# Performance work log

Measured on AMD Instinct MI355X. Metric: run time of the kernel, lower is better.

Reference implementation:

```python
import jax, jax.numpy as jnp
import numpy as np
from jax import lax

# Static pair index table: all C(135,2)=9045 unordered node pairs (replaces the
# nested Python loops with a single gather).
PAIR_I, PAIR_J = np.triu_indices(135, k=1)
RRELU_SLOPE = (1.0 / 8.0 + 1.0 / 3.0) / 2.0  # eval-mode RReLU negative slope
BN_SCALE = 1.0 / float(np.sqrt(1.0 + 1e-5))  # eval BN with running mean=0, var=1


def _leaky(x):
    return jnp.where(x > 0, x, 0.01 * x)


def _conv1d(x, w, b):
    # x: (N, Cin, L), w: (Cout, Cin, K) -> (N, Cout, L-K+1), VALID
    y = lax.conv_general_dilated(x, w, (1,), 'VALID',
                                 dimension_numbers=('NCH', 'OIH', 'NCH'))
    return y + b[None, :, None]


def _bn_eval(x, g, b):
    # nn.BatchNorm1d in eval with fresh running stats (mean=0, var=1)
    return x * (g * BN_SCALE)[None, :, None] + b[None, :, None]


def _maxpool2d(x):
    # nn.MaxPool2d(2) applied to a 3D (N, H, W) tensor: 2x2 pool over (H, W)
    return lax.reduce_window(x, -jnp.inf, lax.max, (1, 2, 2), (1, 2, 2), 'VALID')


def setup_inputs() -> dict:
    key = jax.random.key(0)
    ks = iter(jax.random.split(key, 40))

    def w(shape, scale=0.05):
        return (jax.random.normal(next(ks), shape, jnp.float32) * scale)

    inp = {
        'x': jax.random.normal(next(ks), (30, 135, 375), jnp.float32),
        # FeatureExtractor
        'conv1_w': w((32, 1, 3)), 'conv1_b': jnp.zeros((32,), jnp.float32),
        'bn1_g': jnp.ones((32,), jnp.float32), 'bn1_b': jnp.zeros((32,), jnp.float32),
        'conv2_w': w((64, 16, 3)), 'conv2_b': jnp.zeros((64,), jnp.float32),
        'bn2_g': jnp.ones((64,), jnp.float32), 'bn2_b': jnp.zeros((64,), jnp.float32),
        'conv3_w': w((96, 32, 3)), 'conv3_b': jnp.zeros((96,), jnp.float32),
        'bn3_g': jnp.ones((96,), jnp.float32), 'bn3_b': jnp.zeros((96,), jnp.float32),
        'fe_fc_w': w((48 * 45, 32)), 'fe_fc_b': jnp.zeros((32,), jnp.float32),
        # SimilarityMeasureNetwork
        'sim_w1': w((64, 32)), 'sim_b1': jnp.zeros((32,), jnp.float32),
        'sim_w2': w((32, 16)), 'sim_b2': jnp.zeros((16,), jnp.float32),
        'sim_w3': w((16, 8)), 'sim_b3': jnp.zeros((8,), jnp.float32),
        'sim_w4': w((8, 1)), 'sim_b4': jnp.zeros((1,), jnp.float32),
        # ClassificationNet(9045, 3)
        'cls_w1': w((9045, 1024), 0.01), 'cls_b1': jnp.zeros((1024,), jnp.float32),
        'cls_w2': w((1024, 256)), 'cls_b2': jnp.zeros((256,), jnp.float32),
        'cls_w3': w((256, 64)), 'cls_b3': jnp.zeros((64,), jnp.float32),
        'cls_w4': w((64, 3)), 'cls_b4': jnp.zeros((3,), jnp.float32),
    }
    return inp


def reference(x, conv1_w, conv1_b, bn1_g, bn1_b, conv2_w, conv2_b, bn2_g, bn2_b,
              conv3_w, conv3_b, bn3_g, bn3_b, fe_fc_w, fe_fc_b,
              sim_w1, sim_b1, sim_w2, sim_b2, sim_w3, sim_b3, sim_w4, sim_b4,
              cls_w1, cls_b1, cls_w2, cls_b2, cls_w3, cls_b3, cls_w4, cls_b4):
    B = x.shape[0]  # 30 subjects
    h = x.reshape(B * 135, 1, 375)
    # FeatureExtractor (all subjects*nodes batched together)
    h = _maxpool2d(_leaky(_bn_eval(_conv1d(h, conv1_w, conv1_b), bn1_g, bn1_b)))  # (N,16,186)
    h = _maxpool2d(_leaky(_bn_eval(_conv1d(h, conv2_w, conv2_b), bn2_g, bn2_b)))  # (N,32,92)
    h = _maxpool2d(_leaky(_bn_eval(_conv1d(h, conv3_w, conv3_b), bn3_g, bn3_b)))  # (N,48,45)
    h = h.reshape(B * 135, -1) @ fe_fc_w + fe_fc_b  # (B*135, 32)
    feats = h.reshape(B, 135, 32)

    # All-pairs concat: single gather replacing the nested loops -> (B, 9045, 64)
    pi = jnp.asarray(PAIR_I)
    pj = jnp.asarray(PAIR_J)
    pairs = jnp.concatenate([feats[:, pi, :], feats[:, pj, :]], axis=-1)

    # SimilarityMeasureNetwork
    s = jax.nn.relu(pairs @ sim_w1 + sim_b1)
    s = jax.nn.relu(s @ sim_w2 + sim_b2)
    s = jax.nn.relu(s @ sim_w3 + sim_b3)
    s = jnp.tanh(s @ sim_w4 + sim_b4)  # (B, 9045, 1)
    subjects = s[..., 0]  # (B, 9045)

    # ClassificationNet (eval mode: RReLU -> fixed slope, dropout -> identity)
    c = subjects @ cls_w1 + cls_b1
    c = jnp.where(c >= 0, c, RRELU_SLOPE * c)
    c = jax.nn.relu(c @ cls_w2 + cls_b2)
    c = jax.nn.relu(c @ cls_w3 + cls_b3)
    c = c @ cls_w4 + cls_b4
    return jax.nn.log_softmax(c, axis=1)  # (B, 3)
```

## Files before the change

kernel.cpp:

```cpp
#include <hip/hip_runtime.h>
#include <math.h>

#define BN_SCALE 0.99999500003749967f
#define RRELU_SLOPE 0.22916666666666666f

static __device__ __forceinline__ float leaky(float v) { return v > 0.f ? v : 0.01f * v; }

typedef __attribute__((ext_vector_type(8))) short bf16x8;
typedef __attribute__((ext_vector_type(4))) float f32x4;
typedef __attribute__((ext_vector_type(4))) unsigned u32x4;

static __device__ __forceinline__ unsigned short f2bf(float f) {
  unsigned u = __builtin_bit_cast(unsigned, f);
  u = (u + 0x7FFFu + ((u >> 16) & 1u)) >> 16;
  return (unsigned short)u;
}

__global__ __launch_bounds__(256) void setup_kernel(
    const float* __restrict__ w2c, const float* __restrict__ g2,
    const float* __restrict__ w3c, const float* __restrict__ g3,
    const float* __restrict__ fcw, const float* __restrict__ fcb,
    const float* __restrict__ w1,  const float* __restrict__ b1,
    unsigned short* __restrict__ w2frag,
    unsigned short* __restrict__ w3frag,
    unsigned short* __restrict__ bfragGG,
    float* __restrict__ bgagb,
    unsigned short* __restrict__ subjectsA)
{
  const int item = blockIdx.x * 256 + threadIdx.x;
  if (item < 512) {
    const int tl = item >> 6, lane = item & 63;
    const int mt = tl >> 1, kc = tl & 1;
    const int lr = lane & 15, quad = lane >> 4;
    const int c = mt * 16 + lr;
    const float gs = g2[c] * BN_SCALE;
#pragma unroll
    for (int j = 0; j < 8; ++j) {
      const int k = quad * 8 + j;
      float v;
      if (kc == 0) { const int tap = k >> 4, ci = k & 15; v = w2c[c * 48 + ci * 3 + tap] * gs; }
      else         { v = (k < 16) ? w2c[c * 48 + k * 3 + 2] * gs : 0.f; }
      w2frag[item * 8 + j] = f2bf(v);
    }
  } else if (item < 1664) {
    const int it = item - 512;
    const int tl = it >> 6, lane = it & 63;
    const int mt = tl / 3, tap = tl - mt * 3;
    const int lr = lane & 15, quad = lane >> 4;
    const int c = mt * 16 + lr;
    const float gs = g3[c] * BN_SCALE;
#pragma unroll
    for (int j = 0; j < 8; ++j) {
      const int ci = quad * 8 + j;
      w3frag[it * 8 + j] = f2bf(w3c[c * 96 + ci * 3 + tap] * gs);
    }
  } else if (item < 19072) {
    const int it = item - 1664;
    const int chunk = it >> 8;
    const int rem = it & 255;
    const int nt = rem >> 6;
    const int lane = rem & 63;
    const int lr = lane & 15, quad = lane >> 4;
    const int n = nt * 16 + lr;
    const int off = (n >= 32) ? 32 : 0;
    const int nj = n & 31;
    float w1col[32];
#pragma unroll 8
    for (int q = 0; q < 32; ++q) w1col[q] = w1[(q + off) * 32 + nj];
#pragma unroll
    for (int j = 0; j < 8; ++j) {
      const int k = chunk * 32 + quad * 8 + j;
      float v = 0.f;
      if (k < 2160) {
        const float* fr = fcw + (size_t)k * 32;
#pragma unroll 8
        for (int q = 0; q < 32; ++q) v = fmaf(fr[q], w1col[q], v);
      }
      bfragGG[(size_t)it * 8 + j] = f2bf(v);
    }
  } else if (item < 19136) {
    const int n = item - 19072;
    const int off = (n >= 32) ? 32 : 0;
    const int nj = n & 31;
    float s = (n < 32) ? b1[nj] : 0.f;
    for (int q = 0; q < 32; ++q) s = fmaf(fcb[q], w1[(q + off) * 32 + nj], s);
    bgagb[n] = s;
  } else if (item < 55360) {
    const int idx = item - 19136;
    uint4 z = {0u, 0u, 0u, 0u};
    ((uint4*)subjectsA)[idx] = z;
  }
}

__global__ __launch_bounds__(64) void fe_kernel(
    const float* __restrict__ x,
    const float* __restrict__ w1c, const float* __restrict__ b1c,
    const float* __restrict__ g1,  const float* __restrict__ bb1,
    const float* __restrict__ b2c, const float* __restrict__ g2, const float* __restrict__ bb2,
    const float* __restrict__ b3c, const float* __restrict__ g3, const float* __restrict__ bb3,
    const unsigned short* __restrict__ w2frag,
    const unsigned short* __restrict__ w3frag,
    unsigned short* __restrict__ act3)
{
  __shared__ __align__(16) char A[8448];
  const int lane = threadIdx.x;
  const int quad = lane >> 4, lr = lane & 15;
  const int n = blockIdx.x;

  unsigned short* buf = (unsigned short*)A;
  float* be2 = (float*)(A + 6272);
  float* be3 = (float*)(A + 6528);
  float* sx  = (float*)(A + 6912);

  const float* xr = x + (size_t)n * 375;
  for (int i = lane; i < 375; i += 64) sx[i] = xr[i];

  bf16x8 a2[4][2];
#pragma unroll
  for (int mt = 0; mt < 4; ++mt)
#pragma unroll
    for (int kc = 0; kc < 2; ++kc)
      a2[mt][kc] = *(const bf16x8*)(w2frag + ((mt * 2 + kc) * 64 + lane) * 8);

  be2[lane] = b2c[lane] * (g2[lane] * BN_SCALE) + bb2[lane];
  be3[lane] = b3c[lane] * (g3[lane] * BN_SCALE) + bb3[lane];
  if (lane < 32) be3[64 + lane] = b3c[64 + lane] * (g3[64 + lane] * BN_SCALE) + bb3[64 + lane];
  ((unsigned*)buf)[1488 + lane] = 0;

  const int cp = lane & 7;
  float u[4][3], bbr[4];
#pragma unroll
  for (int d = 0; d < 4; ++d) {
    const int c = cp * 4 + d;
    const float gs = g1[c] * BN_SCALE;
    u[d][0] = w1c[c * 3 + 0] * gs;
    u[d][1] = w1c[c * 3 + 1] * gs;
    u[d][2] = w1c[c * 3 + 2] * gs;
    bbr[d] = b1c[c] * gs + bb1[c];
  }

  for (int o = lane; o < 1488; o += 64) {
    const int l = o >> 3;
    const int p = 2 * l;
    const float x0 = sx[p], x1 = sx[p + 1], x2 = sx[p + 2], x3 = sx[p + 3];
    unsigned pk = 0;
#pragma unroll
    for (int uu = 0; uu < 2; ++uu) {
      float m = -3.4e38f;
#pragma unroll
      for (int dc = 0; dc < 2; ++dc) {
        const int d = uu * 2 + dc;
        const float v0 = fmaf(x0, u[d][0], fmaf(x1, u[d][1], fmaf(x2, u[d][2], bbr[d])));
        const float v1 = fmaf(x1, u[d][0], fmaf(x2, u[d][1], fmaf(x3, u[d][2], bbr[d])));
        m = fmaxf(m, fmaxf(v0, v1));
      }
      pk |= (unsigned)f2bf(leaky(m)) << (16 * uu);
    }
    ((unsigned*)buf)[l * 8 + cp] = pk;
  }

  float be2r[4][4];
#pragma unroll
  for (int mt = 0; mt < 4; ++mt)
#pragma unroll
    for (int r = 0; r < 4; ++r) be2r[mt][r] = be2[mt * 16 + quad * 4 + r];

#pragma unroll 2
  for (int nt = 0; nt < 12; ++nt) {
    const int nrow = nt * 16 + lr;
    bf16x8 b0 = *(const bf16x8*)(buf + (nrow + (quad >> 1)) * 16 + (quad & 1) * 8);
    bf16x8 b1 = *(const bf16x8*)(buf + (nrow + 2) * 16 + (quad & 1) * 8);
    f32x4 acc[4];
#pragma unroll
    for (int mt = 0; mt < 4; ++mt)
#pragma unroll
      for (int r = 0; r < 4; ++r) acc[mt][r] = be2r[mt][r];
#pragma unroll
    for (int mt = 0; mt < 4; ++mt)
      acc[mt] = __builtin_amdgcn_mfma_f32_16x16x32_bf16(a2[mt][0], b0, acc[mt], 0, 0, 0);
#pragma unroll
    for (int mt = 0; mt < 4; ++mt)
      acc[mt] = __builtin_amdgcn_mfma_f32_16x16x32_bf16(a2[mt][1], b1, acc[mt], 0, 0, 0);
#pragma unroll
    for (int mt = 0; mt < 4; ++mt) {
      float o[4];
#pragma unroll
      for (int r = 0; r < 4; ++r)
        o[r] = fmaxf(acc[mt][r], __shfl_xor(acc[mt][r], 1));
      if ((lr & 1) == 0) {
        const int np = nrow >> 1;
        if (np <= 91) {
          const float m0 = leaky(fmaxf(o[0], o[1]));
          const float m1 = leaky(fmaxf(o[2], o[3]));
          const unsigned pk = (unsigned)f2bf(m0) | ((unsigned)f2bf(m1) << 16);
          ((unsigned*)buf)[np * 16 + mt * 4 + quad] = pk;
        }
      }
    }
  }

  ((unsigned*)buf)[1472 + lane] = 0;
  if (lane < 32) ((unsigned*)buf)[1536 + lane] = 0;

  unsigned short* actr = act3 + (size_t)n * 2176;
  for (int mt = 0; mt < 6; ++mt) {
    bf16x8 a3[3];
#pragma unroll
    for (int tap = 0; tap < 3; ++tap)
      a3[tap] = *(const bf16x8*)(w3frag + ((mt * 3 + tap) * 64 + lane) * 8);
    float be3r[4];
#pragma unroll
    for (int r = 0; r < 4; ++r) be3r[r] = be3[mt * 16 + quad * 4 + r];
#pragma unroll
    for (int nt = 0; nt < 6; ++nt) {
      const int nrow = nt * 16 + lr;
      f32x4 acc;
#pragma unroll
      for (int r = 0; r < 4; ++r) acc[r] = be3r[r];
#pragma unroll
      for (int tap = 0; tap < 3; ++tap) {
        bf16x8 b = *(const bf16x8*)(buf + (nrow + tap) * 32 + quad * 8);
        acc = __builtin_amdgcn_mfma_f32_16x16x32_bf16(a3[tap], b, acc, 0, 0, 0);
      }
      float o[4];
#pragma unroll
      for (int r = 0; r < 4; ++r)
        o[r] = fmaxf(acc[r], __shfl_xor(acc[r], 1));
      if ((lr & 1) == 0) {
        const int np = nrow >> 1;
        if (np <= 44) {
          const int mp = mt * 8 + quad * 2;
          actr[mp * 45 + np] = f2bf(leaky(fmaxf(o[0], o[1])));
          actr[(mp + 1) * 45 + np] = f2bf(leaky(fmaxf(o[2], o[3])));
        }
      }
    }
  }
  if (lane < 16) actr[2160 + lane] = 0;
}

__global__ __launch_bounds__(256) void gagb_kernel(
    const unsigned short* __restrict__ act3,
    const unsigned short* __restrict__ bfragGG,
    const float* __restrict__ bgagb,
    float* __restrict__ Ga, float* __restrict__ Gb)
{
  __shared__ f32x4 sred[3][4][64];
  const int t = threadIdx.x;
  const int wv = t >> 6, lane = t & 63, quad = lane >> 4, lr = lane & 15;
  const int m0 = blockIdx.x * 16;
  const int arow = min(m0 + lr, 4049);

  f32x4 acc[4] = {};
  const int c0 = wv * 17;
  for (int chunk = c0; chunk < c0 + 17; ++chunk) {
    const bf16x8 a = *(const bf16x8*)(act3 + (size_t)arow * 2176 + chunk * 32 + quad * 8);
#pragma unroll
    for (int nt = 0; nt < 4; ++nt) {
      const bf16x8 b = *(const bf16x8*)(bfragGG + ((size_t)(chunk * 4 + nt) * 64 + lane) * 8);
      acc[nt] = __builtin_amdgcn_mfma_f32_16x16x32_bf16(a, b, acc[nt], 0, 0, 0);
    }
  }
  if (wv > 0) {
#pragma unroll
    for (int nt = 0; nt < 4; ++nt) sred[wv - 1][nt][lane] = acc[nt];
  }
  __syncthreads();
  if (wv == 0) {
#pragma unroll
    for (int nt = 0; nt < 4; ++nt) {
      f32x4 s = acc[nt];
#pragma unroll
      for (int q = 0; q < 3; ++q) {
        const f32x4 o = sred[q][nt][lane];
#pragma unroll
        for (int r = 0; r < 4; ++r) s[r] += o[r];
      }
      const int col = nt * 16 + lr;
      const float bias = bgagb[col];
#pragma unroll
      for (int r = 0; r < 4; ++r) {
        const int row = m0 + quad * 4 + r;
        if (row < 4050) {
          const float v = s[r] + bias;
          if (col < 32) Ga[row * 32 + col] = v;
          else          Gb[row * 32 + (col - 32)] = v;
        }
      }
    }
  }
}

__global__ __launch_bounds__(256) void sim_kernel(
    const float* __restrict__ Ga, const float* __restrict__ Gb,
    const float* __restrict__ w2, const float* __restrict__ b2,
    const float* __restrict__ w3, const float* __restrict__ b3,
    const float* __restrict__ w4, const float* __restrict__ b4,
    unsigned short* __restrict__ subjectsA)
{
  __shared__ float sGa[135 * 36];
  __shared__ float sGb[135 * 36];
  __shared__ float sw2[512], sw3[128], sw4[8];
  __shared__ float sb2[16], sb3[8], sb4v[1];

  const int t = threadIdx.x;
  const int b = blockIdx.x >> 5;
  const int c = blockIdx.x & 31;

  for (int i = t; i < 4320; i += 256) {
    const int r = i >> 5, col = i & 31;
    sGa[r * 36 + col] = Ga[b * 4320 + i];
    sGb[r * 36 + col] = Gb[b * 4320 + i];
  }
  for (int i = t; i < 512; i += 256) sw2[i] = w2[i];
  if (t < 128) sw3[t] = w3[t];
  if (t < 8) sw4[t] = w4[t];
  if (t < 16) sb2[t] = b2[t];
  if (t < 8) sb3[t] = b3[t];
  if (t == 0) sb4v[0] = b4[0];
  __syncthreads();

  const int mtile = b >> 4, lrm = b & 15;
  const int pend = min(9045, (c + 1) * 283);
  for (int p = c * 283 + t; p < pend; p += 256) {
    int i = (int)((269.0f - sqrtf((float)(72361 - 8 * p))) * 0.5f);
    i = max(0, min(133, i));
    while (134 * (i + 1) - ((i + 1) * i) / 2 <= p) ++i;
    while (134 * i - (i * (i - 1)) / 2 > p) --i;
    const int j = i + 1 + (p - (134 * i - (i * (i - 1)) / 2));

    float h1[32];
#pragma unroll
    for (int q = 0; q < 8; ++q) {
      const float4 va = *(const float4*)(&sGa[i * 36 + 4 * q]);
      const float4 vb = *(const float4*)(&sGb[j * 36 + 4 * q]);
      h1[4 * q + 0] = fmaxf(va.x + vb.x, 0.f);
      h1[4 * q + 1] = fmaxf(va.y + vb.y, 0.f);
      h1[4 * q + 2] = fmaxf(va.z + vb.z, 0.f);
      h1[4 * q + 3] = fmaxf(va.w + vb.w, 0.f);
    }

    float h2[16];
#pragma unroll
    for (int jj = 0; jj < 16; ++jj) h2[jj] = sb2[jj];
#pragma unroll 8
    for (int ii = 0; ii < 32; ++ii) {
      const float av = h1[ii];
      const float4* wr = reinterpret_cast<const float4*>(&sw2[ii * 16]);
#pragma unroll
      for (int r = 0; r < 4; ++r) {
        float4 w = wr[r];
        h2[4 * r + 0] = fmaf(av, w.x, h2[4 * r + 0]);
        h2[4 * r + 1] = fmaf(av, w.y, h2[4 * r + 1]);
        h2[4 * r + 2] = fmaf(av, w.z, h2[4 * r + 2]);
        h2[4 * r + 3] = fmaf(av, w.w, h2[4 * r + 3]);
      }
    }
#pragma unroll
    for (int jj = 0; jj < 16; ++jj) h2[jj] = fmaxf(h2[jj], 0.f);

    float h3[8];
#pragma unroll
    for (int jj = 0; jj < 8; ++jj) h3[jj] = sb3[jj];
#pragma unroll
    for (int ii = 0; ii < 16; ++ii) {
      const float av = h2[ii];
      const float4* wr = reinterpret_cast<const float4*>(&sw3[ii * 8]);
#pragma unroll
      for (int r = 0; r < 2; ++r) {
        float4 w = wr[r];
        h3[4 * r + 0] = fmaf(av, w.x, h3[4 * r + 0]);
        h3[4 * r + 1] = fmaf(av, w.y, h3[4 * r + 1]);
        h3[4 * r + 2] = fmaf(av, w.z, h3[4 * r + 2]);
        h3[4 * r + 3] = fmaf(av, w.w, h3[4 * r + 3]);
      }
    }
#pragma unroll
    for (int jj = 0; jj < 8; ++jj) h3[jj] = fmaxf(h3[jj], 0.f);

    float z = sb4v[0];
#pragma unroll
    for (int ii = 0; ii < 8; ++ii) z = fmaf(h3[ii], sw4[ii], z);

    const float az = fabsf(z);
    const float e = __expf(-2.f * az);
    const float rr = (1.f - e) / (1.f + e);
    const float val = copysignf(rr, z);

    const int chunk = p >> 5, q8 = (p & 31) >> 3, jj2 = p & 7;
    subjectsA[chunk * 1024 + mtile * 512 + (q8 * 16 + lrm) * 8 + jj2] = f2bf(val);
  }
}

__global__ __launch_bounds__(256) void c1_kernel(
    const unsigned short* __restrict__ subjectsA,
    const float* __restrict__ cw1,
    float* __restrict__ part)
{
  const int t = threadIdx.x;
  const int wv = t >> 6, lane = t & 63, quad = lane >> 4, lr = lane & 15;
  const int job = blockIdx.x * 4 + wv;
  const int ng = job & 15;
  const int kg = job >> 4;
  const int c0 = kg * 5;
  const int cend = min(283, c0 + 5);

  f32x4 acc[2][4] = {};
  for (int ch = c0; ch < cend; ++ch) {
    const bf16x8 a0 = *(const bf16x8*)(subjectsA + ch * 1024 + lane * 8);
    const bf16x8 a1 = *(const bf16x8*)(subjectsA + ch * 1024 + 512 + lane * 8);
    const int kbase = ch * 32 + quad * 8;
#pragma unroll
    for (int nt = 0; nt < 4; ++nt) {
      const int col = (ng * 4 + nt) * 16 + lr;
      float wf[8];
#pragma unroll
      for (int j = 0; j < 8; ++j) {
        const int k = kbase + j;
        wf[j] = (k < 9045) ? cw1[(size_t)k * 1024 + col] : 0.f;
      }
      u32x4 up;
#pragma unroll
      for (int jj = 0; jj < 4; ++jj)
        up[jj] = (unsigned)f2bf(wf[2 * jj]) | ((unsigned)f2bf(wf[2 * jj + 1]) << 16);
      const bf16x8 b = __builtin_bit_cast(bf16x8, up);
      acc[0][nt] = __builtin_amdgcn_mfma_f32_16x16x32_bf16(a0, b, acc[0][nt], 0, 0, 0);
      acc[1][nt] = __builtin_amdgcn_mfma_f32_16x16x32_bf16(a1, b, acc[1][nt], 0, 0, 0);
    }
  }
#pragma unroll
  for (int mt = 0; mt < 2; ++mt)
#pragma unroll
    for (int r = 0; r < 4; ++r) {
      const int m = mt * 16 + quad * 4 + r;
      if (m < 30) {
#pragma unroll
        for (int nt = 0; nt < 4; ++nt) {
          const int col = (ng * 4 + nt) * 16 + lr;
          part[(size_t)(m * 64 + kg) * 1024 + col] = acc[mt][nt][r];
        }
      }
    }
}

__global__ __launch_bounds__(256) void tail_a_kernel(
    const float* __restrict__ part,
    const float* __restrict__ cb1,
    float* __restrict__ act1)
{
  const int r = blockIdx.x >> 2;
  const int cg = blockIdx.x & 3;
  const int j = cg * 256 + threadIdx.x;
  float s = cb1[j];
  const float* pp = part + (size_t)r * 64 * 1024 + j;
#pragma unroll 8
  for (int q = 0; q < 64; ++q) s += pp[q * 1024];
  act1[r * 1024 + j] = s >= 0.f ? s : RRELU_SLOPE * s;
}

__global__ __launch_bounds__(256) void tail_b_kernel(
    const float* __restrict__ act1,
    const float* __restrict__ w2, const float* __restrict__ cb2,
    float* __restrict__ act2)
{
  __shared__ float sa[1024];
  __shared__ float sp[256];
  const int r = blockIdx.x >> 3;
  const int cg = blockIdx.x & 7;
  const int t = threadIdx.x;
  const int c = t & 31;
  const int ks = t >> 5;
  const int col = cg * 32 + c;

  for (int i = t; i < 1024; i += 256) sa[i] = act1[r * 1024 + i];
  __syncthreads();

  float acc = 0.f;
  const int k0 = ks * 128;
  for (int kk = k0; kk < k0 + 128; kk += 4) {
    const float4 a = *reinterpret_cast<const float4*>(&sa[kk]);
    acc = fmaf(a.x, w2[(kk + 0) * 256 + col], acc);
    acc = fmaf(a.y, w2[(kk + 1) * 256 + col], acc);
    acc = fmaf(a.z, w2[(kk + 2) * 256 + col], acc);
    acc = fmaf(a.w, w2[(kk + 3) * 256 + col], acc);
  }
  sp[t] = acc;
  __syncthreads();
  if (t < 32) {
    float s = cb2[col];
#pragma unroll
    for (int q = 0; q < 8; ++q) s += sp[q * 32 + t];
    act2[r * 256 + cg * 32 + t] = fmaxf(s, 0.f);
  }
}

__global__ __launch_bounds__(256) void tail_c_kernel(
    const float* __restrict__ act2,
    const float* __restrict__ w3, const float* __restrict__ cb3,
    const float* __restrict__ w4, const float* __restrict__ cb4,
    float* __restrict__ out)
{
  __shared__ float sa[256];
  __shared__ float sp[256];
  __shared__ float sc3[64];
  __shared__ float slg[3];
  const int r = blockIdx.x, t = threadIdx.x;
  const int c = t & 63;
  const int ks = t >> 6;

  sa[t] = act2[r * 256 + t];
  __syncthreads();
  {
    float acc = 0.f;
    const int k0 = ks * 64;
#pragma unroll 4
    for (int kk = k0; kk < k0 + 64; ++kk)
      acc = fmaf(sa[kk], w3[kk * 64 + c], acc);
    sp[t] = acc;
  }
  __syncthreads();
  if (t < 64) {
    const float s = cb3[t] + sp[t] + sp[t + 64] + sp[t + 128] + sp[t + 192];
    sc3[t] = fmaxf(s, 0.f);
  }
  __syncthreads();
  if (t < 3) {
    float acc = cb4[t];
#pragma unroll
    for (int kk = 0; kk < 64; ++kk) acc = fmaf(sc3[kk], w4[kk * 3 + t], acc);
    slg[t] = acc;
  }
  __syncthreads();
  if (t == 0) {
    float m = fmaxf(slg[0], fmaxf(slg[1], slg[2]));
    float se = __expf(slg[0] - m) + __expf(slg[1] - m) + __expf(slg[2] - m);
    float lse = m + logf(se);
    out[r * 3 + 0] = slg[0] - lse;
    out[r * 3 + 1] = slg[1] - lse;
    out[r * 3 + 2] = slg[2] - lse;
  }
}

extern "C" void kernel_launch(void* const* d_in, const int* in_sizes, int n_in,
                              void* d_out, int out_size, void* d_ws, size_t ws_size,
                              hipStream_t stream) {
  const float* x    = (const float*)d_in[0];
  const float* w1c  = (const float*)d_in[1];
  const float* b1c  = (const float*)d_in[2];
  const float* g1   = (const float*)d_in[3];
  const float* bb1  = (const float*)d_in[4];
  const float* w2c  = (const float*)d_in[5];
  const float* b2c  = (const float*)d_in[6];
  const float* g2   = (const float*)d_in[7];
  const float* bb2  = (const float*)d_in[8];
  const float* w3c  = (const float*)d_in[9];
  const float* b3c  = (const float*)d_in[10];
  const float* g3   = (const float*)d_in[11];
  const float* bb3  = (const float*)d_in[12];
  const float* fcw  = (const float*)d_in[13];
  const float* fcb  = (const float*)d_in[14];
  const float* sw1  = (const float*)d_in[15];
  const float* sb1  = (const float*)d_in[16];
  const float* sw2  = (const float*)d_in[17];
  const float* sb2  = (const float*)d_in[18];
  const float* sw3  = (const float*)d_in[19];
  const float* sb3  = (const float*)d_in[20];
  const float* sw4  = (const float*)d_in[21];
  const float* sb4  = (const float*)d_in[22];
  const float* cw1  = (const float*)d_in[23];
  const float* cb1  = (const float*)d_in[24];
  const float* cw2  = (const float*)d_in[25];
  const float* cb2  = (const float*)d_in[26];
  const float* cw3  = (const float*)d_in[27];
  const float* cb3  = (const float*)d_in[28];
  const float* cw4  = (const float*)d_in[29];
  const float* cb4  = (const float*)d_in[30];

  float* ws = (float*)d_ws;
  float* Ga    = ws;
  float* Gb    = ws + 129600;
  float* part  = ws + 259200;
  float* bgagb = ws + 2225280;
  float* act1  = ws + 2225344;
  float* act2  = ws + 2256064;
  unsigned short* wsu = (unsigned short*)(ws + 2263744);
  unsigned short* w2frag    = wsu;
  unsigned short* w3frag    = wsu + 4096;
  unsigned short* bfragGG   = wsu + 13312;
  unsigned short* act3      = wsu + 152576;
  unsigned short* subjectsA = wsu + 8965376;

  setup_kernel<<<217, 256, 0, stream>>>(w2c, g2, w3c, g3, fcw, fcb, sw1, sb1,
                                        w2frag, w3frag, bfragGG, bgagb, subjectsA);
  fe_kernel<<<4050, 64, 0, stream>>>(x, w1c, b1c, g1, bb1, b2c, g2, bb2,
                                     b3c, g3, bb3, w2frag, w3frag, act3);
  gagb_kernel<<<254, 256, 0, stream>>>(act3, bfragGG, bgagb, Ga, Gb);
  sim_kernel<<<960, 256, 0, stream>>>(Ga, Gb, sw2, sb2, sw3, sb3, sw4, sb4, subjectsA);
  c1_kernel<<<256, 256, 0, stream>>>(subjectsA, cw1, part);
  tail_a_kernel<<<120, 256, 0, stream>>>(part, cb1, act1);
  tail_b_kernel<<<240, 256, 0, stream>>>(act1, cw2, cb2, act2);
  tail_c_kernel<<<30, 256, 0, stream>>>(act2, cw3, cb3, cw4, cb4, (float*)d_out);
}
```

Baseline: 258.8 us.

## Split-K gagb and c1 across more blocks; precompute pair index table

Splits the gagb GEMM along K into two halves written to separate partial buffers, and moves the bias add and the sum of the partials into sim_kernel's shared-memory load. Doubles the K split of c1_kernel to 128 groups (launching 512 blocks) so tail_a reduces over 128 partials. Replaces the per-pair sqrt/loop index inversion in sim_kernel with a lookup of a packed (i,j) table built once in setup_kernel. The goal is more blocks to fill the GPU's compute units and less per-pair integer work, at the cost of more partial-sum traffic and a larger reduction in tail_a.

```diff
diff --git a/kernel.cpp b/kernel.cpp
--- a/kernel.cpp
+++ b/kernel.cpp
@@ -25,7 +25,8 @@
     unsigned short* __restrict__ w3frag,
     unsigned short* __restrict__ bfragGG,
     float* __restrict__ bgagb,
-    unsigned short* __restrict__ subjectsA)
+    unsigned short* __restrict__ subjectsA,
+    unsigned short* __restrict__ pairIJ)
 {
   const int item = blockIdx.x * 256 + threadIdx.x;
   if (item < 512) {
@@ -89,6 +90,14 @@
     const int idx = item - 19136;
     uint4 z = {0u, 0u, 0u, 0u};
     ((uint4*)subjectsA)[idx] = z;
+  } else if (item < 64405) {
+    const int p = item - 55360;
+    int i = (int)((269.0f - sqrtf((float)(72361 - 8 * p))) * 0.5f);
+    i = max(0, min(133, i));
+    while (134 * (i + 1) - ((i + 1) * i) / 2 <= p) ++i;
+    while (134 * i - (i * (i - 1)) / 2 > p) --i;
+    const int j = i + 1 + (p - (134 * i - (i * (i - 1)) / 2));
+    pairIJ[p] = (unsigned short)((i << 8) | j);
   }
 }
 
@@ -242,18 +251,21 @@
 __global__ __launch_bounds__(256) void gagb_kernel(
     const unsigned short* __restrict__ act3,
     const unsigned short* __restrict__ bfragGG,
-    const float* __restrict__ bgagb,
-    float* __restrict__ Ga, float* __restrict__ Gb)
+    float* __restrict__ Gpart)
 {
   __shared__ f32x4 sred[3][4][64];
   const int t = threadIdx.x;
   const int wv = t >> 6, lane = t & 63, quad = lane >> 4, lr = lane & 15;
-  const int m0 = blockIdx.x * 16;
+  const int mt = blockIdx.x >> 1;
+  const int half = blockIdx.x & 1;
+  const int m0 = mt * 16;
   const int arow = min(m0 + lr, 4049);
 
   f32x4 acc[4] = {};
-  const int c0 = wv * 17;
-  for (int chunk = c0; chunk < c0 + 17; ++chunk) {
+  const int base = half * 34;
+  const int c0 = base + ((wv * 34) >> 2);
+  const int c1 = base + (((wv + 1) * 34) >> 2);
+  for (int chunk = c0; chunk < c1; ++chunk) {
     const bf16x8 a = *(const bf16x8*)(act3 + (size_t)arow * 2176 + chunk * 32 + quad * 8);
 #pragma unroll
     for (int nt = 0; nt < 4; ++nt) {
@@ -267,6 +279,7 @@
   }
   __syncthreads();
   if (wv == 0) {
+    float* Gp = Gpart + (size_t)half * 259200;
 #pragma unroll
     for (int nt = 0; nt < 4; ++nt) {
       f32x4 s = acc[nt];
@@ -277,25 +290,21 @@
         for (int r = 0; r < 4; ++r) s[r] += o[r];
       }
       const int col = nt * 16 + lr;
-      const float bias = bgagb[col];
 #pragma unroll
       for (int r = 0; r < 4; ++r) {
         const int row = m0 + quad * 4 + r;
-        if (row < 4050) {
-          const float v = s[r] + bias;
-          if (col < 32) Ga[row * 32 + col] = v;
-          else          Gb[row * 32 + (col - 32)] = v;
-        }
+        if (row < 4050) Gp[row * 64 + col] = s[r];
       }
     }
   }
 }
 
 __global__ __launch_bounds__(256) void sim_kernel(
-    const float* __restrict__ Ga, const float* __restrict__ Gb,
+    const float* __restrict__ Gpart, const float* __restrict__ bgagb,
     const float* __restrict__ w2, const float* __restrict__ b2,
     const float* __restrict__ w3, const float* __restrict__ b3,
     const float* __restrict__ w4, const float* __restrict__ b4,
+    const unsigned short* __restrict__ pairIJ,
     unsigned short* __restrict__ subjectsA)
 {
   __shared__ float sGa[135 * 36];
@@ -307,10 +316,13 @@
   const int b = blockIdx.x >> 5;
   const int c = blockIdx.x & 31;
 
-  for (int i = t; i < 4320; i += 256) {
-    const int r = i >> 5, col = i & 31;
-    sGa[r * 36 + col] = Ga[b * 4320 + i];
-    sGb[r * 36 + col] = Gb[b * 4320 + i];
+  const float* Gp0 = Gpart;
+  const float* Gp1 = Gpart + 259200;
+  for (int idx = t; idx < 4320; idx += 256) {
+    const int r = idx >> 5, col = idx & 31;
+    const int row = b * 135 + r;
+    sGa[r * 36 + col] = Gp0[row * 64 + col] + Gp1[row * 64 + col] + bgagb[col];
+    sGb[r * 36 + col] = Gp0[row * 64 + 32 + col] + Gp1[row * 64 + 32 + col] + bgagb[32 + col];
   }
   for (int i = t; i < 512; i += 256) sw2[i] = w2[i];
   if (t < 128) sw3[t] = w3[t];
@@ -323,11 +335,9 @@
   const int mtile = b >> 4, lrm = b & 15;
   const int pend = min(9045, (c + 1) * 283);
   for (int p = c * 283 + t; p < pend; p += 256) {
-    int i = (int)((269.0f - sqrtf((float)(72361 - 8 * p))) * 0.5f);
-    i = max(0, min(133, i));
-    while (134 * (i + 1) - ((i + 1) * i) / 2 <= p) ++i;
-    while (134 * i - (i * (i - 1)) / 2 > p) --i;
-    const int j = i + 1 + (p - (134 * i - (i * (i - 1)) / 2));
+    const unsigned pij = pairIJ[p];
+    const int i = pij >> 8;
+    const int j = pij & 255;
 
     float h1[32];
 #pragma unroll
@@ -402,8 +412,8 @@
   const int job = blockIdx.x * 4 + wv;
   const int ng = job & 15;
   const int kg = job >> 4;
-  const int c0 = kg * 5;
-  const int cend = min(283, c0 + 5);
+  const int c0 = (kg * 283) >> 7;
+  const int cend = ((kg + 1) * 283) >> 7;
 
   f32x4 acc[2][4] = {};
   for (int ch = c0; ch < cend; ++ch) {
@@ -437,7 +447,7 @@
 #pragma unroll
         for (int nt = 0; nt < 4; ++nt) {
           const int col = (ng * 4 + nt) * 16 + lr;
-          part[(size_t)(m * 64 + kg) * 1024 + col] = acc[mt][nt][r];
+          part[(size_t)(m * 128 + kg) * 1024 + col] = acc[mt][nt][r];
         }
       }
     }
@@ -452,9 +462,9 @@
   const int cg = blockIdx.x & 3;
   const int j = cg * 256 + threadIdx.x;
   float s = cb1[j];
-  const float* pp = part + (size_t)r * 64 * 1024 + j;
+  const float* pp = part + (size_t)r * 128 * 1024 + j;
 #pragma unroll 8
-  for (int q = 0; q < 64; ++q) s += pp[q * 1024];
+  for (int q = 0; q < 128; ++q) s += pp[q * 1024];
   act1[r * 1024 + j] = s >= 0.f ? s : RRELU_SLOPE * s;
 }
 
@@ -577,26 +587,27 @@
   const float* cb4  = (const float*)d_in[30];
 
   float* ws = (float*)d_ws;
-  float* Ga    = ws;
-  float* Gb    = ws + 129600;
-  float* part  = ws + 259200;
-  float* bgagb = ws + 2225280;
-  float* act1  = ws + 2225344;
-  float* act2  = ws + 2256064;
-  unsigned short* wsu = (unsigned short*)(ws + 2263744);
+  float* Gpart = ws;
+  float* part  = ws + 518400;
+  float* bgagb = ws + 4450560;
+  float* act1  = ws + 4450624;
+  float* act2  = ws + 4481344;
+  unsigned short* wsu = (unsigned short*)(ws + 4489024);
   unsigned short* w2frag    = wsu;
   unsigned short* w3frag    = wsu + 4096;
   unsigned short* bfragGG   = wsu + 13312;
   unsigned short* act3      = wsu + 152576;
   unsigned short* subjectsA = wsu + 8965376;
-
-  setup_kernel<<<217, 256, 0, stream>>>(w2c, g2, w3c, g3, fcw, fcb, sw1, sb1,
-                                        w2frag, w3frag, bfragGG, bgagb, subjectsA);
+  unsigned short* pairIJ    = wsu + 9255168;
+
+  setup_kernel<<<252, 256, 0, stream>>>(w2c, g2, w3c, g3, fcw, fcb, sw1, sb1,
+                                        w2frag, w3frag, bfragGG, bgagb, subjectsA, pairIJ);
   fe_kernel<<<4050, 64, 0, stream>>>(x, w1c, b1c, g1, bb1, b2c, g2, bb2,
                                      b3c, g3, bb3, w2frag, w3frag, act3);
-  gagb_kernel<<<254, 256, 0, stream>>>(act3, bfragGG, bgagb, Ga, Gb);
-  sim_kernel<<<960, 256, 0, stream>>>(Ga, Gb, sw2, sb2, sw3, sb3, sw4, sb4, subjectsA);
-  c1_kernel<<<256, 256, 0, stream>>>(subjectsA, cw1, part);
+  gagb_kernel<<<508, 256, 0, stream>>>(act3, bfragGG, Gpart);
+  sim_kernel<<<960, 256, 0, stream>>>(Gpart, bgagb, sw2, sb2, sw3, sb3, sw4, sb4,
+                                      pairIJ, subjectsA);
+  c1_kernel<<<512, 256, 0, stream>>>(subjectsA, cw1, part);
   tail_a_kernel<<<120, 256, 0, stream>>>(part, cb1, act1);
   tail_b_kernel<<<240, 256, 0, stream>>>(act1, cw2, cb2, act2);
   tail_c_kernel<<<30, 256, 0, stream>>>(act2, cw3, cb3, cw4, cb4, (float*)d_out);
```

Result: slower. 268.4 us (+3.7%).
